# Performance work log

Hardware: AMD Instinct MI355X
Metric: run time of the kernel (lower is better)

The kernel has to match this reference:

```python
import jax, jax.numpy as jnp
import numpy as np

FS = 16000.0
Q = 2.0
MAX_MFC = 150.0
LP_CUTOFF = 2.5
ATT_FACTOR = 1.0  # dau1997 preset


def _mfc_array():
    # mfc = 0 (lowpass), 5, 10 Hz linear, then log-spaced with ratio r up to max_mfc
    mfc = [0.0, 5.0, 10.0]
    r = (1.0 + 1.0 / (2.0 * Q)) / (1.0 - 1.0 / (2.0 * Q))  # = 5/3 for Q=2
    f = 10.0 * r
    while f <= MAX_MFC:
        mfc.append(f)
        f *= r
    return np.array(mfc, dtype=np.float64)  # 8 entries for the defaults


def _butter2_lp(fcut, fs):
    # 2nd-order Butterworth lowpass via bilinear transform (matches scipy.signal.butter)
    K = np.tan(np.pi * fcut / fs)
    n = 1.0 / (1.0 + np.sqrt(2.0) * K + K * K)
    b = np.array([K * K, 2.0 * K * K, K * K]) * n
    a = np.array([1.0, 2.0 * (K * K - 1.0) * n, (1.0 - np.sqrt(2.0) * K + K * K) * n])
    return b, a


def setup_inputs() -> dict:
    key = jax.random.key(0)
    x = jax.random.normal(key, (4, 31, 48000), dtype=jnp.float32)  # [B, F, T]
    return {"x": x}


def reference(x):
    B, F, T = x.shape
    N = B * F
    xr = x.reshape(N, T)

    # ---- mfc = 0 filter: 2nd-order Butterworth lowpass @ 2.5 Hz, DF2T scan ----
    b_np, a_np = _butter2_lp(LP_CUTOFF, FS)
    b = jnp.asarray(b_np, jnp.float32)
    a = jnp.asarray(a_np, jnp.float32)

    def lp_step(state, xt):  # state [N,2], xt [N]
        y = b[0] * xt + state[:, 0]
        s0 = b[1] * xt - a[1] * y + state[:, 1]
        s1 = b[2] * xt - a[2] * y
        return jnp.stack([s0, s1], axis=1), y

    _, ylp = jax.lax.scan(lp_step, jnp.zeros((N, 2), jnp.float32), xr.T)
    ylp = 2.0 * ylp.T  # [N, T], factor 2 = 6 dB emphasis

    # ---- bandpass efilt: complex first-order resonators ----
    mfc = _mfc_array()[1:]                      # [M] bandpass center freqs
    bw = np.where(mfc <= 10.0, 5.0, mfc / Q)    # 5 Hz bandwidth for linear part
    e0 = np.exp(-np.pi * bw / FS)               # exp(-(2*pi*bw/fs)/2)
    b0 = jnp.asarray((1.0 - e0).astype(np.complex64))
    cpole = jnp.asarray((e0 * np.exp(1j * 2.0 * np.pi * mfc / FS)).astype(np.complex64))
    M = mfc.shape[0]

    def bp_step(yprev, xt):  # yprev [N,M] complex, xt [N] complex
        y = b0[None, :] * xt[:, None] + cpole[None, :] * yprev
        return y, y

    _, ybp = jax.lax.scan(bp_step, jnp.zeros((N, M), jnp.complex64),
                          xr.T.astype(jnp.complex64))
    ybp = 2.0 * jnp.moveaxis(ybp, 0, -1)        # [N, M, T]

    # phase preserved for mfc <= 10 Hz (real part), envelope (abs) above
    keep_phase = jnp.asarray(mfc <= 10.0)
    out_bp = jnp.where(keep_phase[None, :, None], jnp.real(ybp), ATT_FACTOR * jnp.abs(ybp))

    out = jnp.concatenate([ylp[:, None, :], out_bp], axis=1)  # [N, 1+M, T]
    return out.reshape(B, F, 1 + M, T)
```

## Files before the change

### kernel.cpp

```cpp
#include <hip/hip_runtime.h>
#include <cmath>

#define T_LEN 48000
#define L_CHUNK 128
#define N_CHUNKS 375
#define N_ROWS 124
#define SLOTS 1024
#define ROWS_PER_BLK 64
#define XS_STRIDE 132
#define TR_STRIDE 20
#define CBATCH 25
#define NBATCH 15

struct CoefF {
    float lp_b0, lp_b1, lp_b2, lp_a1, lp_a2;
    float bp_b0[7], bp_cr[7], bp_ci[7];
};
struct CoefD {
    double p00, p01, p10, p11;
    double Pr[7], Pi[7];
};

template <bool FINAL>
__global__ __launch_bounds__(512) void mfb_chunk(const float* __restrict__ x,
                                                 CoefF C,
                                                 float2* __restrict__ ws_fin,
                                                 const float2* __restrict__ ws_init,
                                                 float* __restrict__ out) {
    extern __shared__ __align__(16) float smem[];
    float* xs = smem;
    const int t     = threadIdx.x;
    const int j     = blockIdx.y;
    const int n0    = (int)blockIdx.x * ROWS_PER_BLK;
    const int tbase = j * L_CHUNK;

#pragma unroll
    for (int i = 0; i < 4; ++i) {
        int g = i * 512 + t;
        int r = g >> 5, c = (g & 31) * 4;
        int n = n0 + r;
        float4 v = make_float4(0.f, 0.f, 0.f, 0.f);
        if (n < N_ROWS)
            v = *reinterpret_cast<const float4*>(x + (size_t)n * T_LEN + tbase + c);
        *reinterpret_cast<float4*>(xs + r * XS_STRIDE + c) = v;
    }
    __syncthreads();

    const int ch   = t >> 6;
    const int nn   = t & 63;
    const int n    = n0 + nn;
    const int slot = ch * 128 + n;
    const int widx = j * SLOTS + slot;
    float* trw = FINAL ? (smem + ROWS_PER_BLK * XS_STRIDE + ch * (64 * TR_STRIDE)) : nullptr;

    float f_b0, f_b1 = 0.f, f_b2 = 0.f, f_a1 = 0.f, f_a2 = 0.f, f_cr = 0.f, f_ci = 0.f;
    if (ch == 0) {
        f_b0 = C.lp_b0; f_b1 = C.lp_b1; f_b2 = C.lp_b2; f_a1 = C.lp_a1; f_a2 = C.lp_a2;
    } else {
        f_b0 = 0.f;
#pragma unroll
        for (int c = 1; c < 8; ++c)
            if (ch == c) { f_b0 = C.bp_b0[c - 1]; f_cr = C.bp_cr[c - 1]; f_ci = C.bp_ci[c - 1]; }
    }
    const bool kp = (ch <= 2);

    float s0 = 0.f, s1 = 0.f;
    if (FINAL) { float2 u = ws_init[widx]; s0 = u.x; s1 = u.y; }

    for (int b = 0; b < L_CHUNK / 16; ++b) {
        float4 xv4[4];
#pragma unroll
        for (int q = 0; q < 4; ++q)
            xv4[q] = *reinterpret_cast<const float4*>(xs + nn * XS_STRIDE + b * 16 + q * 4);
        const float* xv = reinterpret_cast<const float*>(xv4);

        float buf[16];
        if (ch == 0) {
#pragma unroll
            for (int k = 0; k < 16; ++k) {
                float xvk = xv[k];
                float y  = fmaf(f_b0, xvk, s0);
                s0 = fmaf(f_b1, xvk, fmaf(-f_a1, y, s1));
                s1 = fmaf(f_b2, xvk, -f_a2 * y);
                if (FINAL) buf[k] = 2.0f * y;
            }
        } else {
#pragma unroll
            for (int k = 0; k < 16; ++k) {
                float xvk = xv[k];
                float nyr = fmaf(f_cr, s0, fmaf(-f_ci, s1, f_b0 * xvk));
                float nyi = fmaf(f_cr, s1, f_ci * s0);
                s0 = nyr; s1 = nyi;
                if (FINAL)
                    buf[k] = kp ? 2.0f * nyr : 2.0f * sqrtf(fmaf(nyr, nyr, nyi * nyi));
            }
        }

        if (FINAL) {
            asm volatile("s_waitcnt lgkmcnt(0)" ::: "memory");
            *reinterpret_cast<float4*>(trw + nn * TR_STRIDE + 0)  = make_float4(buf[0], buf[1], buf[2], buf[3]);
            *reinterpret_cast<float4*>(trw + nn * TR_STRIDE + 4)  = make_float4(buf[4], buf[5], buf[6], buf[7]);
            *reinterpret_cast<float4*>(trw + nn * TR_STRIDE + 8)  = make_float4(buf[8], buf[9], buf[10], buf[11]);
            *reinterpret_cast<float4*>(trw + nn * TR_STRIDE + 12) = make_float4(buf[12], buf[13], buf[14], buf[15]);
            asm volatile("s_waitcnt lgkmcnt(0)" ::: "memory");
#pragma unroll
            for (int s = 0; s < 4; ++s) {
                int rr = s * 16 + (nn >> 2);
                int kk = (nn & 3) * 4;
                int nrow = n0 + rr;
                if (nrow < N_ROWS) {
                    float4 v = *reinterpret_cast<const float4*>(trw + rr * TR_STRIDE + kk);
                    *reinterpret_cast<float4*>(out + (size_t)(nrow * 8 + ch) * T_LEN
                                               + tbase + b * 16 + kk) = v;
                }
            }
        }
    }
    if (!FINAL) ws_fin[widx] = make_float2(s0, s1);
}

__global__ __launch_bounds__(256) void mfb_combine(const float2* __restrict__ ws_fin,
                                                   float2* __restrict__ ws_init,
                                                   CoefD D) {
    int s = blockIdx.x * 256 + threadIdx.x;
    if (s >= SLOTS) return;
    int ch = s >> 7;

    double m00, m01, m10, m11;
    if (ch == 0) {
        m00 = D.p00; m01 = D.p01; m10 = D.p10; m11 = D.p11;
    } else {
        double Pr = 0.0, Pi = 0.0;
#pragma unroll
        for (int c = 1; c < 8; ++c) if (ch == c) { Pr = D.Pr[c - 1]; Pi = D.Pi[c - 1]; }
        m00 = Pr; m01 = -Pi; m10 = Pi; m11 = Pr;
    }

    double u0 = 0.0, u1 = 0.0;
    const float2* base = ws_fin + s;
    float2 fa[CBATCH], fb[CBATCH];

    auto LOAD = [&](float2 (&f)[CBATCH], int jbase) {
#pragma unroll
        for (int i = 0; i < CBATCH; ++i) f[i] = base[(size_t)(jbase + i) * SLOTS];
    };
    auto PROC = [&](const float2 (&f)[CBATCH], int jbase) {
#pragma unroll
        for (int i = 0; i < CBATCH; ++i) {
            ws_init[(size_t)(jbase + i) * SLOTS + s] = make_float2((float)u0, (float)u1);
            double t0 = (double)f[i].x + m00 * u0 + m01 * u1;
            double t1 = (double)f[i].y + m10 * u0 + m11 * u1;
            u0 = t0; u1 = t1;
        }
    };

    LOAD(fa, 0);
    for (int bt = 0; bt < NBATCH; bt += 2) {
        if (bt + 1 < NBATCH) LOAD(fb, (bt + 1) * CBATCH);
        PROC(fa, bt * CBATCH);
        if (bt + 2 < NBATCH) LOAD(fa, (bt + 2) * CBATCH);
        if (bt + 1 < NBATCH) PROC(fb, (bt + 1) * CBATCH);
    }
}

extern "C" void kernel_launch(void* const* d_in, const int* in_sizes, int n_in,
                              void* d_out, int out_size, void* d_ws, size_t ws_size,
                              hipStream_t stream) {
    const float* x = (const float*)d_in[0];
    float* out = (float*)d_out;
    char* ws = (char*)d_ws;
    float2* ws_fin  = (float2*)ws;
    float2* ws_init = (float2*)(ws + 3072000);

    const double PI = 3.141592653589793;
    const double FS = 16000.0;
    CoefF C; CoefD D;
    {
        double K   = tan(PI * 2.5 / FS);
        double nrm = 1.0 / (1.0 + sqrt(2.0) * K + K * K);
        double a1  = 2.0 * (K * K - 1.0) * nrm;
        double a2  = (1.0 - sqrt(2.0) * K + K * K) * nrm;
        C.lp_b0 = (float)(K * K * nrm);
        C.lp_b1 = (float)(2.0 * K * K * nrm);
        C.lp_b2 = (float)(K * K * nrm);
        C.lp_a1 = (float)a1;
        C.lp_a2 = (float)a2;
        double p00 = -a1, p01 = 1.0, p10 = -a2, p11 = 0.0;
        for (int i = 0; i < 7; ++i) {
            double q00 = p00 * p00 + p01 * p10, q01 = p00 * p01 + p01 * p11;
            double q10 = p10 * p00 + p11 * p10, q11 = p10 * p01 + p11 * p11;
            p00 = q00; p01 = q01; p10 = q10; p11 = q11;
        }
        D.p00 = p00; D.p01 = p01; D.p10 = p10; D.p11 = p11;

        double r = (1.0 + 1.0 / 4.0) / (1.0 - 1.0 / 4.0);
        double mfc[7]; mfc[0] = 5.0; mfc[1] = 10.0;
        double f = 10.0 * r;
        for (int m = 2; m < 7; ++m) { mfc[m] = f; f *= r; }
        for (int m = 0; m < 7; ++m) {
            double bw = (mfc[m] <= 10.0) ? 5.0 : mfc[m] * 0.5;
            double e0 = exp(-PI * bw / FS);
            double th = 2.0 * PI * mfc[m] / FS;
            C.bp_b0[m] = (float)(1.0 - e0);
            C.bp_cr[m] = (float)(e0 * cos(th));
            C.bp_ci[m] = (float)(e0 * sin(th));
            double eL  = exp(-PI * bw * (double)L_CHUNK / FS);
            double ang = th * (double)L_CHUNK;
            D.Pr[m] = eL * cos(ang);
            D.Pi[m] = eL * sin(ang);
        }
    }

    const int smem1 = ROWS_PER_BLK * XS_STRIDE * 4;
    const int smem3 = smem1 + 8 * 64 * TR_STRIDE * 4;
    dim3 grid(2, N_CHUNKS);
    mfb_chunk<false><<<grid, 512, smem1, stream>>>(x, C, ws_fin, nullptr, nullptr);
    mfb_combine<<<4, 256, 0, stream>>>(ws_fin, ws_init, D);
    mfb_chunk<true><<<grid, 512, smem3, stream>>>(x, C, nullptr, ws_init, out);
}
```

Measured before the change: 85.07 us.

## Fuse three-phase chunked scan into one persistent kernel with grid barriers

Replaces the three launches (chunk-local scan, carry combine, final scan) with one persistent kernel of 250 blocks that loops over tiles and separates the phases with atomic-based grid-wide barriers. The aim is to cut launch overheads and inter-kernel gaps. In exchange it adds a memset launch, the cost of the global barriers, and the combine phase now runs on only two blocks while all other blocks wait. It also depends on all 250 blocks being co-resident, otherwise the barrier deadlocks.

```diff
diff --git a/kernel.cpp b/kernel.cpp
--- a/kernel.cpp
+++ b/kernel.cpp
@@ -11,6 +11,8 @@
 #define TR_STRIDE 20
 #define CBATCH 25
 #define NBATCH 15
+#define NBLK 250
+#define NTILE 750
 
 struct CoefF {
     float lp_b0, lp_b1, lp_b2, lp_a1, lp_a2;
@@ -21,18 +23,37 @@
     double Pr[7], Pi[7];
 };
 
+__device__ __forceinline__ void gbar(unsigned* bar, unsigned nb) {
+    __syncthreads();
+    if (threadIdx.x == 0) {
+        unsigned g = __hip_atomic_load(&bar[1], __ATOMIC_ACQUIRE, __HIP_MEMORY_SCOPE_AGENT);
+        __threadfence();
+        unsigned a = __hip_atomic_fetch_add(&bar[0], 1u, __ATOMIC_ACQ_REL, __HIP_MEMORY_SCOPE_AGENT);
+        if (a == nb - 1u) {
+            __hip_atomic_store(&bar[0], 0u, __ATOMIC_RELAXED, __HIP_MEMORY_SCOPE_AGENT);
+            __hip_atomic_fetch_add(&bar[1], 1u, __ATOMIC_RELEASE, __HIP_MEMORY_SCOPE_AGENT);
+        } else {
+            while (__hip_atomic_load(&bar[1], __ATOMIC_ACQUIRE, __HIP_MEMORY_SCOPE_AGENT) == g)
+                __builtin_amdgcn_s_sleep(8);
+        }
+    }
+    __syncthreads();
+}
+
 template <bool FINAL>
-__global__ __launch_bounds__(512) void mfb_chunk(const float* __restrict__ x,
-                                                 CoefF C,
-                                                 float2* __restrict__ ws_fin,
-                                                 const float2* __restrict__ ws_init,
-                                                 float* __restrict__ out) {
-    extern __shared__ __align__(16) float smem[];
+__device__ __forceinline__ void process_tile(int tau, const float* __restrict__ x,
+                                             const CoefF& C,
+                                             float2* __restrict__ ws_fin,
+                                             const float2* __restrict__ ws_init,
+                                             float* __restrict__ out,
+                                             float* __restrict__ smem) {
     float* xs = smem;
     const int t     = threadIdx.x;
-    const int j     = blockIdx.y;
-    const int n0    = (int)blockIdx.x * ROWS_PER_BLK;
+    const int j     = tau >> 1;
+    const int n0    = (tau & 1) * ROWS_PER_BLK;
     const int tbase = j * L_CHUNK;
+
+    __syncthreads();
 
 #pragma unroll
     for (int i = 0; i < 4; ++i) {
@@ -49,9 +70,8 @@
     const int ch   = t >> 6;
     const int nn   = t & 63;
     const int n    = n0 + nn;
-    const int slot = ch * 128 + n;
-    const int widx = j * SLOTS + slot;
-    float* trw = FINAL ? (smem + ROWS_PER_BLK * XS_STRIDE + ch * (64 * TR_STRIDE)) : nullptr;
+    const int widx = j * SLOTS + ch * 128 + n;
+    float* trw = smem + ROWS_PER_BLK * XS_STRIDE + ch * (64 * TR_STRIDE);
 
     float f_b0, f_b1 = 0.f, f_b2 = 0.f, f_a1 = 0.f, f_a2 = 0.f, f_cr = 0.f, f_ci = 0.f;
     if (ch == 0) {
@@ -119,13 +139,9 @@
     if (!FINAL) ws_fin[widx] = make_float2(s0, s1);
 }
 
-__global__ __launch_bounds__(256) void mfb_combine(const float2* __restrict__ ws_fin,
-                                                   float2* __restrict__ ws_init,
-                                                   CoefD D) {
-    int s = blockIdx.x * 256 + threadIdx.x;
-    if (s >= SLOTS) return;
+__device__ __forceinline__ void combine_body(int s, const float2* __restrict__ ws_fin,
+                                             float2* __restrict__ ws_init, const CoefD& D) {
     int ch = s >> 7;
-
     double m00, m01, m10, m11;
     if (ch == 0) {
         m00 = D.p00; m01 = D.p01; m10 = D.p10; m11 = D.p11;
@@ -161,6 +177,29 @@
         if (bt + 2 < NBATCH) LOAD(fa, (bt + 2) * CBATCH);
         if (bt + 1 < NBATCH) PROC(fb, (bt + 1) * CBATCH);
     }
+}
+
+__global__ __launch_bounds__(512, 2) void mfb_fused(const float* __restrict__ x,
+                                                    CoefF C, CoefD D,
+                                                    float2* __restrict__ ws_fin,
+                                                    float2* __restrict__ ws_init,
+                                                    float* __restrict__ out,
+                                                    unsigned* __restrict__ bar) {
+    extern __shared__ __align__(16) float smem[];
+    const int bid = blockIdx.x;
+
+    for (int tau = bid; tau < NTILE; tau += NBLK)
+        process_tile<false>(tau, x, C, ws_fin, nullptr, nullptr, smem);
+
+    gbar(bar, NBLK);
+
+    if (bid < 2)
+        combine_body(bid * 512 + (int)threadIdx.x, ws_fin, ws_init, D);
+
+    gbar(bar, NBLK);
+
+    for (int tau = bid; tau < NTILE; tau += NBLK)
+        process_tile<true>(tau, x, C, nullptr, ws_init, out, smem);
 }
 
 extern "C" void kernel_launch(void* const* d_in, const int* in_sizes, int n_in,
@@ -171,6 +210,7 @@
     char* ws = (char*)d_ws;
     float2* ws_fin  = (float2*)ws;
     float2* ws_init = (float2*)(ws + 3072000);
+    unsigned* bar   = (unsigned*)(ws + 6144000);
 
     const double PI = 3.141592653589793;
     const double FS = 16000.0;
@@ -211,10 +251,7 @@
         }
     }
 
-    const int smem1 = ROWS_PER_BLK * XS_STRIDE * 4;
-    const int smem3 = smem1 + 8 * 64 * TR_STRIDE * 4;
-    dim3 grid(2, N_CHUNKS);
-    mfb_chunk<false><<<grid, 512, smem1, stream>>>(x, C, ws_fin, nullptr, nullptr);
-    mfb_combine<<<4, 256, 0, stream>>>(ws_fin, ws_init, D);
-    mfb_chunk<true><<<grid, 512, smem3, stream>>>(x, C, nullptr, ws_init, out);
-}
+    const int smem3 = ROWS_PER_BLK * XS_STRIDE * 4 + 8 * 64 * TR_STRIDE * 4;
+    hipMemsetAsync(bar, 0, 8, stream);
+    mfb_fused<<<NBLK, 512, smem3, stream>>>(x, C, D, ws_fin, ws_init, out, bar);
+}
```

After: 326.7 us. 284% more time.

## Split serial chunk-carry combine into hierarchical group-sum, group-scan, expand kernels

Applied to the files above, without the earlier changes.

Replaces the single 4-block sequential carry scan over 375 chunks with a three-level scan: per-group aggregates over 15 chunks (100 blocks), a 25-step scan of group carries using the 15th power of the transition matrices, then a parallel expansion back to per-chunk initial states. This cuts the long serial dependency chain and low-occupancy kernel that dominated the combine step. It adds two extra kernel launches, rereads ws_fin, and introduces float rounding of intermediate group aggregates.

```diff
diff --git a/kernel.cpp b/kernel.cpp
--- a/kernel.cpp
+++ b/kernel.cpp
@@ -9,8 +9,8 @@
 #define ROWS_PER_BLK 64
 #define XS_STRIDE 132
 #define TR_STRIDE 20
-#define CBATCH 25
-#define NBATCH 15
+#define GRP 15
+#define NGRP 25
 
 struct CoefF {
     float lp_b0, lp_b1, lp_b2, lp_a1, lp_a2;
@@ -20,6 +20,18 @@
     double p00, p01, p10, p11;
     double Pr[7], Pi[7];
 };
+
+__device__ __forceinline__ void sel_M(int ch, const CoefD& D,
+                                      double& m00, double& m01, double& m10, double& m11) {
+    if (ch == 0) {
+        m00 = D.p00; m01 = D.p01; m10 = D.p10; m11 = D.p11;
+    } else {
+        double Pr = 0.0, Pi = 0.0;
+#pragma unroll
+        for (int c = 1; c < 8; ++c) if (ch == c) { Pr = D.Pr[c - 1]; Pi = D.Pi[c - 1]; }
+        m00 = Pr; m01 = -Pi; m10 = Pi; m11 = Pr;
+    }
+}
 
 template <bool FINAL>
 __global__ __launch_bounds__(512) void mfb_chunk(const float* __restrict__ x,
@@ -49,9 +61,8 @@
     const int ch   = t >> 6;
     const int nn   = t & 63;
     const int n    = n0 + nn;
-    const int slot = ch * 128 + n;
-    const int widx = j * SLOTS + slot;
-    float* trw = FINAL ? (smem + ROWS_PER_BLK * XS_STRIDE + ch * (64 * TR_STRIDE)) : nullptr;
+    const int widx = j * SLOTS + ch * 128 + n;
+    float* trw = smem + ROWS_PER_BLK * XS_STRIDE + ch * (64 * TR_STRIDE);
 
     float f_b0, f_b1 = 0.f, f_b2 = 0.f, f_a1 = 0.f, f_a2 = 0.f, f_cr = 0.f, f_ci = 0.f;
     if (ch == 0) {
@@ -119,47 +130,69 @@
     if (!FINAL) ws_fin[widx] = make_float2(s0, s1);
 }
 
-__global__ __launch_bounds__(256) void mfb_combine(const float2* __restrict__ ws_fin,
-                                                   float2* __restrict__ ws_init,
-                                                   CoefD D) {
-    int s = blockIdx.x * 256 + threadIdx.x;
-    if (s >= SLOTS) return;
-    int ch = s >> 7;
-
+__global__ __launch_bounds__(256) void mfb_groupsum(const float2* __restrict__ ws_fin,
+                                                    float2* __restrict__ A, CoefD D) {
+    int tid = blockIdx.x * 256 + (int)threadIdx.x;
+    int s = tid & 1023, g = tid >> 10;
     double m00, m01, m10, m11;
-    if (ch == 0) {
-        m00 = D.p00; m01 = D.p01; m10 = D.p10; m11 = D.p11;
-    } else {
-        double Pr = 0.0, Pi = 0.0;
-#pragma unroll
-        for (int c = 1; c < 8; ++c) if (ch == c) { Pr = D.Pr[c - 1]; Pi = D.Pi[c - 1]; }
-        m00 = Pr; m01 = -Pi; m10 = Pi; m11 = Pr;
-    }
+    sel_M(s >> 7, D, m00, m01, m10, m11);
+
+    const float2* base = ws_fin + (size_t)g * GRP * SLOTS + s;
+    float2 f[GRP];
+#pragma unroll
+    for (int i = 0; i < GRP; ++i) f[i] = base[(size_t)i * SLOTS];
+
+    double a0 = 0.0, a1 = 0.0;
+#pragma unroll
+    for (int i = 0; i < GRP; ++i) {
+        double t0 = m00 * a0 + m01 * a1 + (double)f[i].x;
+        double t1 = m10 * a0 + m11 * a1 + (double)f[i].y;
+        a0 = t0; a1 = t1;
+    }
+    A[(size_t)g * SLOTS + s] = make_float2((float)a0, (float)a1);
+}
+
+__global__ __launch_bounds__(256) void mfb_groupscan(const float2* __restrict__ A,
+                                                     float2* __restrict__ U, CoefD D15) {
+    int s = blockIdx.x * 256 + (int)threadIdx.x;
+    double m00, m01, m10, m11;
+    sel_M(s >> 7, D15, m00, m01, m10, m11);
+
+    float2 f[NGRP];
+#pragma unroll
+    for (int g = 0; g < NGRP; ++g) f[g] = A[(size_t)g * SLOTS + s];
 
     double u0 = 0.0, u1 = 0.0;
-    const float2* base = ws_fin + s;
-    float2 fa[CBATCH], fb[CBATCH];
-
-    auto LOAD = [&](float2 (&f)[CBATCH], int jbase) {
-#pragma unroll
-        for (int i = 0; i < CBATCH; ++i) f[i] = base[(size_t)(jbase + i) * SLOTS];
-    };
-    auto PROC = [&](const float2 (&f)[CBATCH], int jbase) {
-#pragma unroll
-        for (int i = 0; i < CBATCH; ++i) {
-            ws_init[(size_t)(jbase + i) * SLOTS + s] = make_float2((float)u0, (float)u1);
-            double t0 = (double)f[i].x + m00 * u0 + m01 * u1;
-            double t1 = (double)f[i].y + m10 * u0 + m11 * u1;
-            u0 = t0; u1 = t1;
-        }
-    };
-
-    LOAD(fa, 0);
-    for (int bt = 0; bt < NBATCH; bt += 2) {
-        if (bt + 1 < NBATCH) LOAD(fb, (bt + 1) * CBATCH);
-        PROC(fa, bt * CBATCH);
-        if (bt + 2 < NBATCH) LOAD(fa, (bt + 2) * CBATCH);
-        if (bt + 1 < NBATCH) PROC(fb, (bt + 1) * CBATCH);
+#pragma unroll
+    for (int g = 0; g < NGRP; ++g) {
+        U[(size_t)g * SLOTS + s] = make_float2((float)u0, (float)u1);
+        double t0 = (double)f[g].x + m00 * u0 + m01 * u1;
+        double t1 = (double)f[g].y + m10 * u0 + m11 * u1;
+        u0 = t0; u1 = t1;
+    }
+}
+
+__global__ __launch_bounds__(256) void mfb_expand(const float2* __restrict__ ws_fin,
+                                                  const float2* __restrict__ U,
+                                                  float2* __restrict__ ws_init, CoefD D) {
+    int tid = blockIdx.x * 256 + (int)threadIdx.x;
+    int s = tid & 1023, g = tid >> 10;
+    double m00, m01, m10, m11;
+    sel_M(s >> 7, D, m00, m01, m10, m11);
+
+    const float2* base = ws_fin + (size_t)g * GRP * SLOTS + s;
+    float2 f[GRP];
+#pragma unroll
+    for (int i = 0; i < GRP; ++i) f[i] = base[(size_t)i * SLOTS];
+
+    float2 ug = U[(size_t)g * SLOTS + s];
+    double u0 = ug.x, u1 = ug.y;
+#pragma unroll
+    for (int i = 0; i < GRP; ++i) {
+        ws_init[(size_t)(g * GRP + i) * SLOTS + s] = make_float2((float)u0, (float)u1);
+        double t0 = (double)f[i].x + m00 * u0 + m01 * u1;
+        double t1 = (double)f[i].y + m10 * u0 + m11 * u1;
+        u0 = t0; u1 = t1;
     }
 }
 
@@ -171,10 +204,12 @@
     char* ws = (char*)d_ws;
     float2* ws_fin  = (float2*)ws;
     float2* ws_init = (float2*)(ws + 3072000);
+    float2* Agg     = (float2*)(ws + 6144000);
+    float2* Upre    = (float2*)(ws + 6348800);
 
     const double PI = 3.141592653589793;
     const double FS = 16000.0;
-    CoefF C; CoefD D;
+    CoefF C; CoefD D, D15;
     {
         double K   = tan(PI * 2.5 / FS);
         double nrm = 1.0 / (1.0 + sqrt(2.0) * K + K * K);
@@ -192,11 +227,23 @@
             p00 = q00; p01 = q01; p10 = q10; p11 = q11;
         }
         D.p00 = p00; D.p01 = p01; D.p10 = p10; D.p11 = p11;
-
-        double r = (1.0 + 1.0 / 4.0) / (1.0 - 1.0 / 4.0);
+        double r00 = 1, r01 = 0, r10 = 0, r11 = 1, b00 = p00, b01 = p01, b10 = p10, b11 = p11;
+        for (int e = 15; e > 0; e >>= 1) {
+            if (e & 1) {
+                double q00 = r00 * b00 + r01 * b10, q01 = r00 * b01 + r01 * b11;
+                double q10 = r10 * b00 + r11 * b10, q11 = r10 * b01 + r11 * b11;
+                r00 = q00; r01 = q01; r10 = q10; r11 = q11;
+            }
+            double q00 = b00 * b00 + b01 * b10, q01 = b00 * b01 + b01 * b11;
+            double q10 = b10 * b00 + b11 * b10, q11 = b10 * b01 + b11 * b11;
+            b00 = q00; b01 = q01; b10 = q10; b11 = q11;
+        }
+        D15.p00 = r00; D15.p01 = r01; D15.p10 = r10; D15.p11 = r11;
+
+        double rr = (1.0 + 1.0 / 4.0) / (1.0 - 1.0 / 4.0);
         double mfc[7]; mfc[0] = 5.0; mfc[1] = 10.0;
-        double f = 10.0 * r;
-        for (int m = 2; m < 7; ++m) { mfc[m] = f; f *= r; }
+        double f = 10.0 * rr;
+        for (int m = 2; m < 7; ++m) { mfc[m] = f; f *= rr; }
         for (int m = 0; m < 7; ++m) {
             double bw = (mfc[m] <= 10.0) ? 5.0 : mfc[m] * 0.5;
             double e0 = exp(-PI * bw / FS);
@@ -208,6 +255,10 @@
             double ang = th * (double)L_CHUNK;
             D.Pr[m] = eL * cos(ang);
             D.Pi[m] = eL * sin(ang);
+            double eG  = exp(-PI * bw * (double)(L_CHUNK * GRP) / FS);
+            double angG = th * (double)(L_CHUNK * GRP);
+            D15.Pr[m] = eG * cos(angG);
+            D15.Pi[m] = eG * sin(angG);
         }
     }
 
@@ -215,6 +266,8 @@
     const int smem3 = smem1 + 8 * 64 * TR_STRIDE * 4;
     dim3 grid(2, N_CHUNKS);
     mfb_chunk<false><<<grid, 512, smem1, stream>>>(x, C, ws_fin, nullptr, nullptr);
-    mfb_combine<<<4, 256, 0, stream>>>(ws_fin, ws_init, D);
+    mfb_groupsum<<<100, 256, 0, stream>>>(ws_fin, Agg, D);
+    mfb_groupscan<<<4, 256, 0, stream>>>(Agg, Upre, D15);
+    mfb_expand<<<100, 256, 0, stream>>>(ws_fin, Upre, ws_init, D);
     mfb_chunk<true><<<grid, 512, smem3, stream>>>(x, C, nullptr, ws_init, out);
 }
```

Result: faster. 70.79 us (-16.8%).
